# Kernel tuning notes

Hardware: AMD Instinct MI355X
Metric: run time of the kernel (lower is better)

Reference implementation:

```python
import jax, jax.numpy as jnp
import numpy as np

B, N, K = 4, 4096, 9
EPS = 1e-5

def _bn(y, g, b, axes):
    # BatchNorm forward with batch statistics; channel axis = 1
    m = y.mean(axis=axes, keepdims=True)
    v = y.var(axis=axes, keepdims=True)
    shape = [1] * y.ndim
    shape[1] = -1
    return (y - m) * jax.lax.rsqrt(v + EPS) * g.reshape(shape) + b.reshape(shape)

def _knn(x, k):
    # x: (B, C, N) -> neighbor indices (B, N, k), self-loops excluded
    x2 = jnp.sum(x * x, axis=1)  # (B, N)
    d = x2[:, :, None] + x2[:, None, :] - 2.0 * jnp.einsum('bcn,bcm->bnm', x, x)
    n = d.shape[-1]
    d = d + jnp.eye(n, dtype=d.dtype) * 1e10  # exclude self (self_loop=False)
    return jax.lax.top_k(-d, k)[1]  # (B, N, k)

def _edge_conv(x, idx, w, g, b):
    # EdgeConv: edge feature [x_i, x_j - x_i] -> 1x1 conv -> BN -> ReLU -> max over neighbors
    # x: (B, C, N); idx: (B, N, K); w: (O, 2C)
    xj = jnp.take_along_axis(x[:, :, None, :], idx[:, None, :, :], axis=3)  # (B,C,N,K)
    xi = x[:, :, :, None]
    e = jnp.concatenate([jnp.broadcast_to(xi, xj.shape), xj - xi], axis=1)  # (B,2C,N,K)
    y = jnp.einsum('oc,bcnk->bonk', w, e)
    y = jax.nn.relu(_bn(y, g, b, (0, 2, 3)))
    return y.max(axis=3)  # (B, O, N)

def setup_inputs():
    key = jax.random.key(0)
    ks = jax.random.split(key, 10)
    rn = lambda k, s: jax.random.normal(k, s, dtype=jnp.float32) * 0.1
    return {
        'x': jax.random.normal(ks[0], (B, 3, N), dtype=jnp.float32),
        'coords': jax.random.normal(ks[1], (B, 3, N), dtype=jnp.float32),
        'w1': rn(ks[2], (64, 6)), 'g1': jnp.ones(64), 'b1': jnp.zeros(64),
        'w2': rn(ks[3], (128, 128)), 'g2': jnp.ones(128), 'b2': jnp.zeros(128),
        'w3': rn(ks[4], (256, 256)), 'g3': jnp.ones(256), 'b3': jnp.zeros(256),
        'w4': rn(ks[5], (256, 512)), 'g4': jnp.ones(256), 'b4': jnp.zeros(256),
        'dec_w': rn(ks[6], (48, 64)), 'dec_g': jnp.ones(48), 'dec_b': jnp.zeros(48),
        'fus_w': rn(ks[7], (256, 304)),
        'cls_w1': rn(ks[8], (256, 512)), 'cls_g': jnp.ones(256), 'cls_b': jnp.zeros(256),
        'cls_w2': rn(ks[9], (40, 256)),
    }

def reference(x, coords, w1, g1, b1, w2, g2, b2, w3, g3, b3, w4, g4, b4,
              dec_w, dec_g, dec_b, fus_w, cls_w1, cls_g, cls_b, cls_w2):
    idx = _knn(x, K)                            # graph built once from input coords
    out1 = _edge_conv(x, idx, w1, g1, b1)       # (B, 64, N)  low_level_feats
    out = _edge_conv(out1, idx, w2, g2, b2)     # (B, 128, N)
    out = _edge_conv(out, idx, w3, g3, b3)      # (B, 256, N)
    out = _edge_conv(out, idx, w4, g4, b4)      # (B, 256, N)
    # Decoder (coords is accepted but unused, as in the torch module)
    low = jax.nn.relu(_bn(jnp.einsum('oc,bcn->bon', dec_w, out1), dec_g, dec_b, (0, 2)))  # (B,48,N)
    fused = jnp.einsum('oc,bcn->bon', fus_w, jnp.concatenate([out, low], axis=1))          # (B,256,N)
    h = jnp.concatenate([fused.max(axis=2, keepdims=True),
                         fused.mean(axis=2, keepdims=True)], axis=1)                        # (B,512,1)
    h = jax.nn.relu(_bn(jnp.einsum('oc,bcn->bon', cls_w1, h), cls_g, cls_b, (0, 2)))       # (B,256,1)
    logits = jnp.einsum('oc,bcn->bon', cls_w2, h).squeeze(-1)                               # (B,40)
    return logits
```

## Files before the change

kernel.cpp:

```cpp
#include <hip/hip_runtime.h>

#define BB 4
#define NN 4096
#define KK 9
#define NPTS (BB * NN)
#define EPSF 1e-5f

typedef short short8 __attribute__((ext_vector_type(8)));
typedef float f32x4 __attribute__((ext_vector_type(4)));

__device__ __forceinline__ unsigned short f2bf(float f) {
    unsigned u = __float_as_uint(f);
    unsigned r = (u + 0x7fffu + ((u >> 16) & 1u)) >> 16;
    return (unsigned short)r;
}
__device__ __forceinline__ float bf2f(unsigned short h) {
    return __uint_as_float(((unsigned)h) << 16);
}
__device__ __forceinline__ unsigned fmapu(float f) {
    unsigned u = __float_as_uint(f);
    return (u & 0x80000000u) ? ~u : (u | 0x80000000u);
}
__device__ __forceinline__ float funmap(unsigned m) {
    return (m & 0x80000000u) ? __uint_as_float(m & 0x7fffffffu) : __uint_as_float(~m);
}


__global__ __launch_bounds__(256) void knn_kernel(const float4* __restrict__ xt4, int* __restrict__ idx) {
    __shared__ float4 tile[32][9];
    __shared__ float smin[8][33];
    __shared__ float stauf[8];
    __shared__ int scnt[8];
    __shared__ unsigned long long spk[8][128];
    int tid = threadIdx.x;
    int q = tid & 7;
    int ch = tid >> 3;
    int blk = blockIdx.x;
    int b = blk >> 9;
    int qbase = (blk & 511) << 3;
    int n = qbase + q;
    const float4* xb = xt4 + (b << 12);
    float4 p = xb[n];
    float px2 = -2.0f * p.x, py2 = -2.0f * p.y, pz2 = -2.0f * p.z;
    if (tid < 8) scnt[tid] = 0;

    int lch = tid >> 3, li = tid & 7;
    float mn = 3.0e38f;

    for (int t0 = 0; t0 < 4096; t0 += 256) {
        __syncthreads();
        tile[lch][li] = xb[t0 + tid];
        __syncthreads();
        int mbase = t0 + ch * 8;
#pragma unroll
        for (int i = 0; i < 8; i += 4) {
            float4 c0 = tile[ch][i];
            float4 c1 = tile[ch][i + 1];
            float4 c2 = tile[ch][i + 2];
            float4 c3 = tile[ch][i + 3];
            float d0 = fmaf(px2, c0.x, fmaf(py2, c0.y, fmaf(pz2, c0.z, p.w + c0.w)));
            float d1 = fmaf(px2, c1.x, fmaf(py2, c1.y, fmaf(pz2, c1.z, p.w + c1.w)));
            float d2 = fmaf(px2, c2.x, fmaf(py2, c2.y, fmaf(pz2, c2.z, p.w + c2.w)));
            float d3 = fmaf(px2, c3.x, fmaf(py2, c3.y, fmaf(pz2, c3.z, p.w + c3.w)));
            int m = mbase + i;
            d0 = (m == n) ? 3.0e37f : d0;
            d1 = (m + 1 == n) ? 3.0e37f : d1;
            d2 = (m + 2 == n) ? 3.0e37f : d2;
            d3 = (m + 3 == n) ? 3.0e37f : d3;
            mn = fminf(mn, fminf(fminf(d0, d1), fminf(d2, d3)));
        }
    }
    smin[q][ch] = mn;
    __syncthreads();

    {
        int r = 0;
#pragma unroll 8
        for (int c = 0; c < 32; c++) {
            float u = smin[q][c];
            r += (u < mn || (u == mn && c < ch)) ? 1 : 0;
        }
        if (r == 8) stauf[q] = mn;
    }
    __syncthreads();
    float tau = stauf[q];

    for (int t0 = 0; t0 < 4096; t0 += 256) {
        __syncthreads();
        tile[lch][li] = xb[t0 + tid];
        __syncthreads();
        int mbase = t0 + ch * 8;
#pragma unroll
        for (int i = 0; i < 8; i += 4) {
            float4 c0 = tile[ch][i];
            float4 c1 = tile[ch][i + 1];
            float4 c2 = tile[ch][i + 2];
            float4 c3 = tile[ch][i + 3];
            float d0 = fmaf(px2, c0.x, fmaf(py2, c0.y, fmaf(pz2, c0.z, p.w + c0.w)));
            float d1 = fmaf(px2, c1.x, fmaf(py2, c1.y, fmaf(pz2, c1.z, p.w + c1.w)));
            float d2 = fmaf(px2, c2.x, fmaf(py2, c2.y, fmaf(pz2, c2.z, p.w + c2.w)));
            float d3 = fmaf(px2, c3.x, fmaf(py2, c3.y, fmaf(pz2, c3.z, p.w + c3.w)));
            int m = mbase + i;
            d0 = (m == n) ? 3.0e37f : d0;
            d1 = (m + 1 == n) ? 3.0e37f : d1;
            d2 = (m + 2 == n) ? 3.0e37f : d2;
            d3 = (m + 3 == n) ? 3.0e37f : d3;
            if (fminf(fminf(d0, d1), fminf(d2, d3)) <= tau) {
                if (d0 <= tau) {
                    int slot = atomicAdd(&scnt[q], 1);
                    if (slot < 128)
                        spk[q][slot] = (((unsigned long long)__float_as_uint(fmaxf(d0, 0.f))) << 32) | (unsigned)(m);
                }
                if (d1 <= tau) {
                    int slot = atomicAdd(&scnt[q], 1);
                    if (slot < 128)
                        spk[q][slot] = (((unsigned long long)__float_as_uint(fmaxf(d1, 0.f))) << 32) | (unsigned)(m + 1);
                }
                if (d2 <= tau) {
                    int slot = atomicAdd(&scnt[q], 1);
                    if (slot < 128)
                        spk[q][slot] = (((unsigned long long)__float_as_uint(fmaxf(d2, 0.f))) << 32) | (unsigned)(m + 2);
                }
                if (d3 <= tau) {
                    int slot = atomicAdd(&scnt[q], 1);
                    if (slot < 128)
                        spk[q][slot] = (((unsigned long long)__float_as_uint(fmaxf(d3, 0.f))) << 32) | (unsigned)(m + 3);
                }
            }
        }
    }
    __syncthreads();

    int cnt = scnt[q];
    cnt = (cnt > 128) ? 128 : cnt;
    size_t obase = ((size_t)(b << 12) + qbase + q) * KK;
    for (int s = ch; s < cnt; s += 32) {
        unsigned long long e = spk[q][s];
        int r = 0;
        for (int c = 0; c < cnt; c++) r += (spk[q][c] < e) ? 1 : 0;
        if (r < KK) idx[obase + r] = (int)(unsigned)e;
    }
}

__global__ void wprep_all_kernel(const float* __restrict__ x, const float* __restrict__ w1,
                                 const float* __restrict__ w2, const float* __restrict__ w3,
                                 const float* __restrict__ w4, const float* __restrict__ fw,
                                 float4* __restrict__ xt4,
                                 float* __restrict__ wc1, float* __restrict__ wc2,
                                 unsigned short* __restrict__ wc3h, unsigned short* __restrict__ wc3l,
                                 unsigned short* __restrict__ wc4h, unsigned short* __restrict__ wc4l,
                                 unsigned short* __restrict__ fwh, unsigned short* __restrict__ fwl,
                                 double* __restrict__ stats, unsigned* __restrict__ pmaxU,
                                 double* __restrict__ psum) {
    int i0 = blockIdx.x * 256 + threadIdx.x;
    if (i0 < 96256) stats[i0] = 0.0;
    if (i0 < 1024) { pmaxU[i0] = 0u; psum[i0] = 0.0; }
    int i = i0;
    if (i < 192) {
        int o = i / 3, c = i - o * 3;
        float a = w1[o * 6 + c], b = w1[o * 6 + 3 + c];
        wc1[o * 3 + c] = a - b;
        wc1[(64 + o) * 3 + c] = b;
        return;
    }
    i -= 192;
    if (i < 8192) {
        int o = i / 64, c = i - o * 64;
        float a = w2[o * 128 + c], b = w2[o * 128 + 64 + c];
        wc2[o * 64 + c] = a - b;
        wc2[(128 + o) * 64 + c] = b;
        return;
    }
    i -= 8192;
    if (i < 32768) {
        int o = i / 128, c = i - o * 128;
        float a = w3[o * 256 + c], b = w3[o * 256 + 128 + c];
        float vA = a - b;
        unsigned short h = f2bf(vA);
        wc3h[o * 128 + c] = h;
        wc3l[o * 128 + c] = f2bf(vA - bf2f(h));
        unsigned short h2 = f2bf(b);
        wc3h[(size_t)(256 + o) * 128 + c] = h2;
        wc3l[(size_t)(256 + o) * 128 + c] = f2bf(b - bf2f(h2));
        return;
    }
    i -= 32768;
    if (i < 65536) {
        int o = i / 256, c = i - o * 256;
        float a = w4[o * 512 + c], b = w4[o * 512 + 256 + c];
        float vA = a - b;
        unsigned short h = f2bf(vA);
        wc4h[o * 256 + c] = h;
        wc4l[o * 256 + c] = f2bf(vA - bf2f(h));
        unsigned short h2 = f2bf(b);
        wc4h[(size_t)(256 + o) * 256 + c] = h2;
        wc4l[(size_t)(256 + o) * 256 + c] = f2bf(b - bf2f(h2));
        return;
    }
    i -= 65536;
    if (i < 81920) {
        int o = i / 320, c = i - o * 320;
        float v = (c < 304) ? fw[o * 304 + c] : 0.f;
        unsigned short h = f2bf(v);
        fwh[i] = h;
        fwl[i] = f2bf(v - bf2f(h));
        return;
    }
    i -= 81920;
    if (i < NPTS) {
        int b = i >> 12, n = i & 4095;
        float x0 = x[(b * 3 + 0) * NN + n];
        float x1 = x[(b * 3 + 1) * NN + n];
        float x2 = x[(b * 3 + 2) * NN + n];
        float s = x0 * x0 + x1 * x1 + x2 * x2;
        xt4[i] = make_float4(x0, x1, x2, s);
    }
}

template <int K_, int LDA>
__global__ __launch_bounds__(256) void gemm_kernel(const float* __restrict__ A,
                                                   const float* __restrict__ Bw,
                                                   float* __restrict__ OutB,
                                                   unsigned short* __restrict__ OutZ,
                                                   int CBASE, int ldoB, int ldoZ) {
    constexpr int BK = 16;
    constexpr int LDS_S = 132;
    __shared__ float sA[BK * LDS_S];
    __shared__ float sB[BK * LDS_S];
    int tid = threadIdx.x;
    int m0 = blockIdx.x * 128;
    int n0 = blockIdx.y * 128;
    int lrow = tid >> 2;
    int kq = (tid & 3) * 4;
    int tm = (tid & 15) * 8;
    int tn = (tid >> 4) * 8;

    float acc[8][8];
#pragma unroll
    for (int i = 0; i < 8; i++)
#pragma unroll
        for (int j = 0; j < 8; j++) acc[i][j] = 0.f;

    for (int k0 = 0; k0 < K_; k0 += BK) {
#pragma unroll
        for (int h = 0; h < 2; h++) {
            int r = lrow + h * 64;
            float4 va = *(const float4*)(A + (size_t)(m0 + r) * LDA + k0 + kq);
            sA[(kq + 0) * LDS_S + r] = va.x;
            sA[(kq + 1) * LDS_S + r] = va.y;
            sA[(kq + 2) * LDS_S + r] = va.z;
            sA[(kq + 3) * LDS_S + r] = va.w;
            float4 vb = *(const float4*)(Bw + (size_t)(n0 + r) * K_ + k0 + kq);
            sB[(kq + 0) * LDS_S + r] = vb.x;
            sB[(kq + 1) * LDS_S + r] = vb.y;
            sB[(kq + 2) * LDS_S + r] = vb.z;
            sB[(kq + 3) * LDS_S + r] = vb.w;
        }
        __syncthreads();
#pragma unroll 4
        for (int k = 0; k < BK; k++) {
            float4 a0 = *(const float4*)(sA + k * LDS_S + tm);
            float4 a1 = *(const float4*)(sA + k * LDS_S + tm + 4);
            float4 b0 = *(const float4*)(sB + k * LDS_S + tn);
            float4 b1 = *(const float4*)(sB + k * LDS_S + tn + 4);
            float av[8] = {a0.x, a0.y, a0.z, a0.w, a1.x, a1.y, a1.z, a1.w};
            float bv[8] = {b0.x, b0.y, b0.z, b0.w, b1.x, b1.y, b1.z, b1.w};
#pragma unroll
            for (int i = 0; i < 8; i++)
#pragma unroll
                for (int j = 0; j < 8; j++) acc[i][j] = fmaf(av[i], bv[j], acc[i][j]);
        }
        __syncthreads();
    }
    if (n0 < CBASE) {
#pragma unroll
        for (int i = 0; i < 8; i++) {
            float4 o0 = make_float4(acc[i][0], acc[i][1], acc[i][2], acc[i][3]);
            float4 o1 = make_float4(acc[i][4], acc[i][5], acc[i][6], acc[i][7]);
            float* orow = OutB + (size_t)(m0 + tm + i) * ldoB + n0 + tn;
            *(float4*)(orow) = o0;
            *(float4*)(orow + 4) = o1;
        }
    } else {
        int zc = n0 - CBASE;
#pragma unroll
        for (int i = 0; i < 8; i++) {
            unsigned* zrow = (unsigned*)(OutZ + (size_t)(m0 + tm + i) * ldoZ + zc + tn);
#pragma unroll
            for (int j = 0; j < 4; j++)
                zrow[j] = (unsigned)f2bf(acc[i][2 * j]) | ((unsigned)f2bf(acc[i][2 * j + 1]) << 16);
        }
    }
}

template <int K_>
__global__ __launch_bounds__(256) void gemm_mfma2_kernel(const unsigned short* __restrict__ Ah,
                                                         const unsigned short* __restrict__ Al,
                                                         const unsigned short* __restrict__ Bh,
                                                         const unsigned short* __restrict__ Bl,
                                                         float* __restrict__ OutB,
                                                         unsigned short* __restrict__ OutZ,
                                                         int CBASE, int ldoB, int ldoZ) {
    constexpr int LR = 40;
    __shared__ unsigned short sAh[128 * LR];
    __shared__ unsigned short sAl[128 * LR];
    __shared__ unsigned short sBh[128 * LR];
    __shared__ unsigned short sBl[128 * LR];
    int tid = threadIdx.x;
    int wave = tid >> 6, lane = tid & 63;
    int r16 = lane & 15, quad = lane >> 4;
    int wm = (wave & 1) << 6, wn = (wave >> 1) << 6;
    int m0 = blockIdx.x * 128;
    int n0 = blockIdx.y * 128;
    int sr0 = tid >> 2;
    int sp0 = (tid & 3) * 8;
    const unsigned short* gAh = Ah + (size_t)(m0 + sr0) * K_ + sp0;
    const unsigned short* gAl = Al + (size_t)(m0 + sr0) * K_ + sp0;
    const unsigned short* gBh = Bh + (size_t)(n0 + sr0) * K_ + sp0;
    const unsigned short* gBl = Bl + (size_t)(n0 + sr0) * K_ + sp0;
    const size_t gstep = (size_t)64 * K_;
    unsigned short* lA0h = sAh + sr0 * LR + sp0;
    unsigned short* lA1h = lA0h + 64 * LR;
    unsigned short* lA0l = sAl + sr0 * LR + sp0;
    unsigned short* lA1l = lA0l + 64 * LR;
    unsigned short* lB0h = sBh + sr0 * LR + sp0;
    unsigned short* lB1h = lB0h + 64 * LR;
    unsigned short* lB0l = sBl + sr0 * LR + sp0;
    unsigned short* lB1l = lB0l + 64 * LR;

    f32x4 acc[4][4];
#pragma unroll
    for (int i = 0; i < 4; i++)
#pragma unroll
        for (int j = 0; j < 4; j++) acc[i][j] = (f32x4){0.f, 0.f, 0.f, 0.f};

    for (int k0 = 0; k0 < K_; k0 += 32) {
        __syncthreads();
        *(short8*)lA0h = *(const short8*)(gAh + k0);
        *(short8*)lA1h = *(const short8*)(gAh + gstep + k0);
        *(short8*)lA0l = *(const short8*)(gAl + k0);
        *(short8*)lA1l = *(const short8*)(gAl + gstep + k0);
        *(short8*)lB0h = *(const short8*)(gBh + k0);
        *(short8*)lB1h = *(const short8*)(gBh + gstep + k0);
        *(short8*)lB0l = *(const short8*)(gBl + k0);
        *(short8*)lB1l = *(const short8*)(gBl + gstep + k0);
        __syncthreads();
        short8 bh[4], bl[4];
#pragma unroll
        for (int j = 0; j < 4; j++) {
            bh[j] = *(const short8*)(sBh + (wn + j * 16 + r16) * LR + quad * 8);
            bl[j] = *(const short8*)(sBl + (wn + j * 16 + r16) * LR + quad * 8);
        }
#pragma unroll
        for (int i = 0; i < 4; i++) {
            short8 ah = *(const short8*)(sAh + (wm + i * 16 + r16) * LR + quad * 8);
            short8 al = *(const short8*)(sAl + (wm + i * 16 + r16) * LR + quad * 8);
#pragma unroll
            for (int j = 0; j < 4; j++) {
                acc[i][j] = __builtin_amdgcn_mfma_f32_16x16x32_bf16(ah, bh[j], acc[i][j], 0, 0, 0);
                acc[i][j] = __builtin_amdgcn_mfma_f32_16x16x32_bf16(ah, bl[j], acc[i][j], 0, 0, 0);
                acc[i][j] = __builtin_amdgcn_mfma_f32_16x16x32_bf16(al, bh[j], acc[i][j], 0, 0, 0);
            }
        }
    }

    int orow = quad * 4;
    if (n0 < CBASE) {
#pragma unroll
        for (int i = 0; i < 4; i++) {
#pragma unroll
            for (int v = 0; v < 4; v++) {
                float* prow = OutB + (size_t)(m0 + wm + i * 16 + orow + v) * ldoB + n0 + wn + r16;
#pragma unroll
                for (int j = 0; j < 4; j++) prow[j * 16] = acc[i][j][v];
            }
        }
    } else {
        int zc = n0 - CBASE;
#pragma unroll
        for (int i = 0; i < 4; i++) {
#pragma unroll
            for (int v = 0; v < 4; v++) {
                unsigned short* prow = OutZ + (size_t)(m0 + wm + i * 16 + orow + v) * ldoZ + zc + wn + r16;
#pragma unroll
                for (int j = 0; j < 4; j++) prow[j * 16] = f2bf(acc[i][j][v]);
            }
        }
    }
}

template <int K_>
__global__ __launch_bounds__(256) void gemm_mfma_red2_kernel(const unsigned short* __restrict__ Ah,
                                                             const unsigned short* __restrict__ Al,
                                                             const unsigned short* __restrict__ Bh,
                                                             const unsigned short* __restrict__ Bl,
                                                             unsigned* __restrict__ pmaxU,
                                                             double* __restrict__ psum) {
    constexpr int LR = 40;
    __shared__ unsigned short sAh[128 * LR];
    __shared__ unsigned short sAl[128 * LR];
    __shared__ unsigned short sBh[128 * LR];
    __shared__ unsigned short sBl[128 * LR];
    int tid = threadIdx.x;
    int wave = tid >> 6, lane = tid & 63;
    int r16 = lane & 15, quad = lane >> 4;
    int wm = (wave & 1) << 6, wn = (wave >> 1) << 6;
    int m0 = blockIdx.x * 128;
    int n0 = blockIdx.y * 128;
    int sr0 = tid >> 2;
    int sp0 = (tid & 3) * 8;
    const unsigned short* gAh = Ah + (size_t)(m0 + sr0) * K_ + sp0;
    const unsigned short* gAl = Al + (size_t)(m0 + sr0) * K_ + sp0;
    const unsigned short* gBh = Bh + (size_t)(n0 + sr0) * K_ + sp0;
    const unsigned short* gBl = Bl + (size_t)(n0 + sr0) * K_ + sp0;
    const size_t gstep = (size_t)64 * K_;
    unsigned short* lA0h = sAh + sr0 * LR + sp0;
    unsigned short* lA1h = lA0h + 64 * LR;
    unsigned short* lA0l = sAl + sr0 * LR + sp0;
    unsigned short* lA1l = lA0l + 64 * LR;
    unsigned short* lB0h = sBh + sr0 * LR + sp0;
    unsigned short* lB1h = lB0h + 64 * LR;
    unsigned short* lB0l = sBl + sr0 * LR + sp0;
    unsigned short* lB1l = lB0l + 64 * LR;

    f32x4 acc[4][4];
#pragma unroll
    for (int i = 0; i < 4; i++)
#pragma unroll
        for (int j = 0; j < 4; j++) acc[i][j] = (f32x4){0.f, 0.f, 0.f, 0.f};

    for (int k0 = 0; k0 < K_; k0 += 32) {
        __syncthreads();
        *(short8*)lA0h = *(const short8*)(gAh + k0);
        *(short8*)lA1h = *(const short8*)(gAh + gstep + k0);
        *(short8*)lA0l = *(const short8*)(gAl + k0);
        *(short8*)lA1l = *(const short8*)(gAl + gstep + k0);
        *(short8*)lB0h = *(const short8*)(gBh + k0);
        *(short8*)lB1h = *(const short8*)(gBh + gstep + k0);
        *(short8*)lB0l = *(const short8*)(gBl + k0);
        *(short8*)lB1l = *(const short8*)(gBl + gstep + k0);
        __syncthreads();
        short8 bh[4], bl[4];
#pragma unroll
        for (int j = 0; j < 4; j++) {
            bh[j] = *(const short8*)(sBh + (wn + j * 16 + r16) * LR + quad * 8);
            bl[j] = *(const short8*)(sBl + (wn + j * 16 + r16) * LR + quad * 8);
        }
#pragma unroll
        for (int i = 0; i < 4; i++) {
            short8 ah = *(const short8*)(sAh + (wm + i * 16 + r16) * LR + quad * 8);
            short8 al = *(const short8*)(sAl + (wm + i * 16 + r16) * LR + quad * 8);
#pragma unroll
            for (int j = 0; j < 4; j++) {
                acc[i][j] = __builtin_amdgcn_mfma_f32_16x16x32_bf16(ah, bh[j], acc[i][j], 0, 0, 0);
                acc[i][j] = __builtin_amdgcn_mfma_f32_16x16x32_bf16(ah, bl[j], acc[i][j], 0, 0, 0);
                acc[i][j] = __builtin_amdgcn_mfma_f32_16x16x32_bf16(al, bh[j], acc[i][j], 0, 0, 0);
            }
        }
    }

    int batch = (blockIdx.x * 128) >> 12;
#pragma unroll
    for (int j = 0; j < 4; j++) {
        float mx = -3.0e38f, sm = 0.f;
#pragma unroll
        for (int i = 0; i < 4; i++) {
#pragma unroll
            for (int v = 0; v < 4; v++) {
                float val = acc[i][j][v];
                mx = fmaxf(mx, val);
                sm += val;
            }
        }
        mx = fmaxf(mx, __shfl_xor(mx, 16));
        mx = fmaxf(mx, __shfl_xor(mx, 32));
        sm += __shfl_xor(sm, 16);
        sm += __shfl_xor(sm, 32);
        if (quad == 0) {
            int col = n0 + wn + j * 16 + r16;
            atomicMax(&pmaxU[batch * 256 + col], fmapu(mx));
            atomicAdd(&psum[batch * 256 + col], (double)sm);
        }
    }
}

__global__ __launch_bounds__(256) void gather1_kernel(const float4* __restrict__ xt4,
                                                      const int* __restrict__ idxb,
                                                      const float* __restrict__ wc1,
                                                      float* __restrict__ ymax,
                                                      double* __restrict__ stats) {
    __shared__ float swc[384];
    __shared__ float reds[4][64], reds2[4][64];
    int tid = threadIdx.x;
    for (int e = tid; e < 384; e += 256) swc[e] = wc1[e];
    __syncthreads();
    int t = tid & 63, p = tid >> 6;
    int n = blockIdx.x * 4 + p;
    int bbase = n & ~4095;
    float4 xn = xt4[n];
    float4 xj[KK];
#pragma unroll
    for (int k = 0; k < KK; k++) {
        int nbk = bbase + idxb[n * KK + k];
        xj[k] = xt4[nbk];
    }
    float a0 = swc[t * 3], a1 = swc[t * 3 + 1], a2 = swc[t * 3 + 2];
    float b0 = swc[(64 + t) * 3], b1 = swc[(64 + t) * 3 + 1], b2 = swc[(64 + t) * 3 + 2];
    float base = xn.x * a0 + xn.y * a1 + xn.z * a2;
    float mx = -3.0e38f, s = 0.f, s2 = 0.f;
#pragma unroll
    for (int k = 0; k < KK; k++) {
        float z = xj[k].x * b0 + xj[k].y * b1 + xj[k].z * b2;
        float v = base + z;
        mx = fmaxf(mx, v);
        s += v;
        s2 += v * v;
    }
    ymax[(size_t)n * 64 + t] = mx;
    reds[p][t] = s;
    reds2[p][t] = s2;
    __syncthreads();
    if (p == 0) {
        double ds = (double)reds[0][t] + (double)reds[1][t] + (double)reds[2][t] + (double)reds[3][t];
        double ds2 = (double)reds2[0][t] + (double)reds2[1][t] + (double)reds2[2][t] + (double)reds2[3][t];
        int part = blockIdx.x & 63;
        atomicAdd(&stats[part * 64 + t], ds);
        atomicAdd(&stats[64 * 64 + part * 64 + t], ds2);
    }
}

template <int COUT>
__global__ __launch_bounds__(256) void gather_kernel(const float* __restrict__ Gb,
                                                     const unsigned short* __restrict__ Gz,
                                                     const int* __restrict__ idxb,
                                                     float* __restrict__ ymax,
                                                     double* __restrict__ stats) {
    __shared__ float reds[4][64], reds2[4][64];
    int t = threadIdx.x & 63;
    int p = threadIdx.x >> 6;
    int blk = blockIdx.x;
    int xcd = blk & 7, grp = blk >> 3;
    int batch = xcd >> 1;
    int n = (batch << 12) + (((grp << 1) | (xcd & 1)) << 2) + p;
    int bbase = n & ~4095;
    int nb[KK];
#pragma unroll
    for (int k = 0; k < KK; k++) nb[k] = bbase + idxb[n * KK + k];
    const float* gb = Gb + (size_t)n * COUT;
    int part = blk & 63;
#pragma unroll 1
    for (int u = 0; u < COUT / 64; u++) {
        int o = t + u * 64;
        float base = gb[o];
        float mx = -3.0e38f, s = 0.f, s2 = 0.f;
#pragma unroll
        for (int k = 0; k < KK; k++) {
            float v = base + bf2f(Gz[(size_t)nb[k] * COUT + o]);
            mx = fmaxf(mx, v);
            s += v;
            s2 += v * v;
        }
        ymax[(size_t)n * COUT + o] = mx;
        reds[p][t] = s;
        reds2[p][t] = s2;
        __syncthreads();
        if (p == 0) {
            double ds = (double)reds[0][t] + (double)reds[1][t] + (double)reds[2][t] + (double)reds[3][t];
            double ds2 = (double)reds2[0][t] + (double)reds2[1][t] + (double)reds2[2][t] + (double)reds2[3][t];
            atomicAdd(&stats[part * COUT + o], ds);
            atomicAdd(&stats[64 * COUT + part * COUT + o], ds2);
        }
        __syncthreads();
    }
}

template <int COUT>
__global__ void finalize_kernel(const double* __restrict__ stats, const float* __restrict__ g,
                                const float* __restrict__ bias, float* __restrict__ ss,
                                float count) {
    int o = threadIdx.x;
    if (o >= COUT) return;
    double s = 0.0, s2 = 0.0;
    for (int p = 0; p < 64; p++) {
        s += stats[p * COUT + o];
        s2 += stats[64 * COUT + p * COUT + o];
    }
    double m = s / (double)count;
    double var = s2 / (double)count - m * m;
    float scale = g[o] * rsqrtf((float)var + EPSF);
    ss[o] = scale;
    ss[COUT + o] = bias[o] - (float)m * scale;
}

__global__ __launch_bounds__(256) void apply1dec_kernel(const float* __restrict__ ymax,
                                                        const float* __restrict__ ss,
                                                        const float* __restrict__ decw,
                                                        float* __restrict__ act1, float* __restrict__ z,
                                                        double* __restrict__ stats) {
    __shared__ __align__(16) float sx[4][64];
    __shared__ float sz[4][48];
    int t = threadIdx.x & 63, p = threadIdx.x >> 6;
    int n = blockIdx.x * 4 + p;
    size_t i = (size_t)n * 64 + t;
    float s = ss[t], sh = ss[64 + t];
    float r = fmaxf(fmaf(s, ymax[i], sh), 0.f);
    act1[i] = r;
    sx[p][t] = r;
    __syncthreads();
    if (t < 48) {
        const float* wr = decw + t * 64;
        float acc = 0.f;
#pragma unroll
        for (int c = 0; c < 64; c += 4) {
            float4 wv = *(const float4*)(wr + c);
            float4 xv = *(const float4*)(&sx[p][c]);
            acc += wv.x * xv.x + wv.y * xv.y + wv.z * xv.z + wv.w * xv.w;
        }
        z[(size_t)n * 48 + t] = acc;
        sz[p][t] = acc;
    }
    __syncthreads();
    if (p == 0 && t < 48) {
        double ds = 0.0, ds2 = 0.0;
#pragma unroll
        for (int pp = 0; pp < 4; pp++) {
            double a = (double)sz[pp][t];
            ds += a;
            ds2 += a * a;
        }
        int part = blockIdx.x & 63;
        atomicAdd(&stats[part * 48 + t], ds);
        atomicAdd(&stats[64 * 48 + part * 48 + t], ds2);
    }
}

template <int COUT, int LDO>
__global__ void apply_split_kernel(const float* __restrict__ ymax, const float* __restrict__ ss,
                                   unsigned short* __restrict__ outh,
                                   unsigned short* __restrict__ outl) {
    int i = blockIdx.x * 256 + threadIdx.x;
    int o = i & (COUT - 1);
    int n = i / COUT;
    float s = ss[o], sh = ss[COUT + o];
    float r = fmaxf(fmaf(s, ymax[i], sh), 0.f);
    unsigned short h = f2bf(r);
    size_t a = (size_t)n * LDO + o;
    outh[a] = h;
    outl[a] = f2bf(r - bf2f(h));
}

__global__ __launch_bounds__(320) void applyfused_kernel(const float* __restrict__ ymax,
                                                         const float* __restrict__ ss4,
                                                         const float* __restrict__ zdec,
                                                         const float* __restrict__ ssD,
                                                         unsigned short* __restrict__ fh,
                                                         unsigned short* __restrict__ fl) {
    int n = blockIdx.x;
    int o = threadIdx.x;
    float r = 0.f;
    if (o < 256) {
        float s = ss4[o], sh = ss4[256 + o];
        r = fmaxf(fmaf(s, ymax[(size_t)n * 256 + o], sh), 0.f);
    } else if (o < 304) {
        int oo = o - 256;
        float s = ssD[oo], sh = ssD[48 + oo];
        r = fmaxf(fmaf(s, zdec[(size_t)n * 48 + oo], sh), 0.f);
    }
    unsigned short h = f2bf(r);
    size_t a = (size_t)n * 320 + o;
    fh[a] = h;
    fl[a] = f2bf(r - bf2f(h));
}

__global__ __launch_bounds__(256) void cls1_kernel(const unsigned* __restrict__ pmaxU,
                                                   const double* __restrict__ psum,
                                                   const float* __restrict__ w1,
                                                   const float* __restrict__ g,
                                                   const float* __restrict__ bias,
                                                   float* __restrict__ h2o) {
    __shared__ __align__(16) float sh[4 * 512];
    __shared__ float red[16][17][4];
    int tid = threadIdx.x;
    int c = tid >> 4;
    int seg = tid & 15;
#pragma unroll
    for (int i = 0; i < 8; i++) {
        int e = tid + i * 256;
        int b2 = e >> 9, o = e & 511;
        sh[e] = (o < 256) ? funmap(pmaxU[b2 * 256 + o])
                          : (float)(psum[b2 * 256 + (o - 256)] * (1.0 / 4096.0));
    }
    __syncthreads();
    int t = blockIdx.x * 16 + c;
    const float* wr = w1 + (size_t)t * 512 + seg * 4;
    float a0 = 0.f, a1 = 0.f, a2 = 0.f, a3 = 0.f;
#pragma unroll
    for (int j = 0; j < 8; j++) {
        float4 wv = *(const float4*)(wr + j * 64);
        int so = seg * 4 + j * 64;
        float4 s0 = *(const float4*)(&sh[0 * 512 + so]);
        float4 s1 = *(const float4*)(&sh[1 * 512 + so]);
        float4 s2 = *(const float4*)(&sh[2 * 512 + so]);
        float4 s3 = *(const float4*)(&sh[3 * 512 + so]);
        a0 += wv.x * s0.x + wv.y * s0.y + wv.z * s0.z + wv.w * s0.w;
        a1 += wv.x * s1.x + wv.y * s1.y + wv.z * s1.z + wv.w * s1.w;
        a2 += wv.x * s2.x + wv.y * s2.y + wv.z * s2.z + wv.w * s2.w;
        a3 += wv.x * s3.x + wv.y * s3.y + wv.z * s3.z + wv.w * s3.w;
    }
    red[c][seg][0] = a0;
    red[c][seg][1] = a1;
    red[c][seg][2] = a2;
    red[c][seg][3] = a3;
    __syncthreads();
    if (seg == 0) {
        float y[4];
#pragma unroll
        for (int b2 = 0; b2 < 4; b2++) {
            float s = 0.f;
#pragma unroll
            for (int ss = 0; ss < 16; ss++) s += red[c][ss][b2];
            y[b2] = s;
        }
        float m = 0.25f * (y[0] + y[1] + y[2] + y[3]);
        float v = 0.25f * ((y[0] - m) * (y[0] - m) + (y[1] - m) * (y[1] - m) +
                           (y[2] - m) * (y[2] - m) + (y[3] - m) * (y[3] - m));
        float sc = g[t] * rsqrtf(v + EPSF);
        float shf = bias[t] - m * sc;
#pragma unroll
        for (int b2 = 0; b2 < 4; b2++) h2o[b2 * 256 + t] = fmaxf(fmaf(sc, y[b2], shf), 0.f);
    }
}

__global__ __launch_bounds__(256) void cls2_kernel(const float* __restrict__ h2o,
                                                   const float* __restrict__ w2,
                                                   float* __restrict__ out) {
    __shared__ __align__(16) float sh2[4 * 256];
    int t = threadIdx.x;
#pragma unroll
    for (int i = 0; i < 4; i++) sh2[t + i * 256] = h2o[t + i * 256];
    __syncthreads();
    if (t < 160) {
        int b2 = t / 40, j = t % 40;
        const float* wr2 = w2 + j * 256;
        float acc = 0.f;
        for (int c = 0; c < 256; c += 4) {
            float4 wv = *(const float4*)(wr2 + c);
            acc += wv.x * sh2[b2 * 256 + c] + wv.y * sh2[b2 * 256 + c + 1] +
                   wv.z * sh2[b2 * 256 + c + 2] + wv.w * sh2[b2 * 256 + c + 3];
        }
        out[b2 * 40 + j] = acc;
    }
}

extern "C" void kernel_launch(void* const* d_in, const int* in_sizes, int n_in,
                              void* d_out, int out_size, void* d_ws, size_t ws_size,
                              hipStream_t stream) {
    const float* x = (const float*)d_in[0];
    const float* w1 = (const float*)d_in[2];
    const float* g1 = (const float*)d_in[3];
    const float* b1 = (const float*)d_in[4];
    const float* w2 = (const float*)d_in[5];
    const float* g2 = (const float*)d_in[6];
    const float* b2 = (const float*)d_in[7];
    const float* w3 = (const float*)d_in[8];
    const float* g3 = (const float*)d_in[9];
    const float* b3 = (const float*)d_in[10];
    const float* w4 = (const float*)d_in[11];
    const float* g4 = (const float*)d_in[12];
    const float* b4 = (const float*)d_in[13];
    const float* dec_w = (const float*)d_in[14];
    const float* dec_g = (const float*)d_in[15];
    const float* dec_b = (const float*)d_in[16];
    const float* fus_w = (const float*)d_in[17];
    const float* cls_w1 = (const float*)d_in[18];
    const float* cls_g = (const float*)d_in[19];
    const float* cls_b = (const float*)d_in[20];
    const float* cls_w2 = (const float*)d_in[21];
    float* out = (float*)d_out;

    char* ws = (char*)d_ws;
    size_t cur = 0;
    auto alloc = [&](size_t bytes) -> void* {
        void* p = ws + cur;
        cur += (bytes + 255) & ~(size_t)255;
        return p;
    };
    const size_t STATS_DBL = 96256;
    double* stats = (double*)alloc(STATS_DBL * 8);
    const size_t OFF1 = 0, OFF2 = 8192, OFF3 = 24576, OFF4 = 57344, OFFD = 90112;
    double* psum2 = (double*)alloc(1024 * 8);
    unsigned* pmaxU = (unsigned*)alloc(1024 * 4);
    float* h2ws = (float*)alloc(1024 * 4);
    float4* xt4 = (float4*)alloc((size_t)NPTS * 16);
    int* idx = (int*)alloc((size_t)NPTS * KK * 4);
    float* act1 = (float*)alloc((size_t)NPTS * 64 * 4);
    unsigned short* act2h = (unsigned short*)alloc((size_t)NPTS * 128 * 2);
    unsigned short* act2l = (unsigned short*)alloc((size_t)NPTS * 128 * 2);
    unsigned short* act3h = (unsigned short*)alloc((size_t)NPTS * 256 * 2);
    unsigned short* act3l = (unsigned short*)alloc((size_t)NPTS * 256 * 2);
    unsigned short* actfh = (unsigned short*)alloc((size_t)NPTS * 320 * 2);
    unsigned short* actfl = (unsigned short*)alloc((size_t)NPTS * 320 * 2);
    float* Gb = (float*)alloc((size_t)NPTS * 256 * 4);
    unsigned short* Gz = (unsigned short*)alloc((size_t)NPTS * 256 * 2);
    float* zdec = (float*)alloc((size_t)NPTS * 48 * 4);
    float* ymax = (float*)alloc((size_t)NPTS * 256 * 4);
    float* ss = (float*)alloc(2048 * 4);
    const size_t SS1 = 0, SS2 = 128, SS3 = 384, SS4 = 896, SSD = 1408;
    float* wc1 = (float*)alloc(128 * 3 * 4);
    float* wc2 = (float*)alloc(256 * 64 * 4);
    unsigned short* wc3h = (unsigned short*)alloc((size_t)512 * 128 * 2);
    unsigned short* wc3l = (unsigned short*)alloc((size_t)512 * 128 * 2);
    unsigned short* wc4h = (unsigned short*)alloc((size_t)512 * 256 * 2);
    unsigned short* wc4l = (unsigned short*)alloc((size_t)512 * 256 * 2);
    unsigned short* fwh = (unsigned short*)alloc((size_t)256 * 320 * 2);
    unsigned short* fwl = (unsigned short*)alloc((size_t)256 * 320 * 2);

    wprep_all_kernel<<<801, 256, 0, stream>>>(x, w1, w2, w3, w4, fus_w, xt4, wc1, wc2, wc3h, wc3l,
                                              wc4h, wc4l, fwh, fwl, stats, pmaxU, psum2);
    knn_kernel<<<NPTS / 8, 256, 0, stream>>>(xt4, idx);

    gather1_kernel<<<NPTS / 4, 256, 0, stream>>>(xt4, idx, wc1, ymax, stats + OFF1);
    finalize_kernel<64><<<1, 64, 0, stream>>>(stats + OFF1, g1, b1, ss + SS1, 147456.f);
    apply1dec_kernel<<<NPTS / 4, 256, 0, stream>>>(ymax, ss + SS1, dec_w, act1, zdec, stats + OFFD);
    finalize_kernel<48><<<1, 64, 0, stream>>>(stats + OFFD, dec_g, dec_b, ss + SSD, 16384.f);

    gemm_kernel<64, 64><<<dim3(128, 2), 256, 0, stream>>>(act1, wc2, Gb, Gz, 128, 128, 128);
    gather_kernel<128><<<NPTS / 4, 256, 0, stream>>>(Gb, Gz, idx, ymax, stats + OFF2);
    finalize_kernel<128><<<1, 128, 0, stream>>>(stats + OFF2, g2, b2, ss + SS2, 147456.f);
    apply_split_kernel<128, 128><<<NPTS * 128 / 256, 256, 0, stream>>>(ymax, ss + SS2, act2h, act2l);

    gemm_mfma2_kernel<128><<<dim3(128, 4), 256, 0, stream>>>(act2h, act2l, wc3h, wc3l, Gb, Gz,
                                                             256, 256, 256);
    gather_kernel<256><<<NPTS / 4, 256, 0, stream>>>(Gb, Gz, idx, ymax, stats + OFF3);
    finalize_kernel<256><<<1, 256, 0, stream>>>(stats + OFF3, g3, b3, ss + SS3, 147456.f);
    apply_split_kernel<256, 256><<<NPTS * 256 / 256, 256, 0, stream>>>(ymax, ss + SS3, act3h, act3l);

    gemm_mfma2_kernel<256><<<dim3(128, 4), 256, 0, stream>>>(act3h, act3l, wc4h, wc4l, Gb, Gz,
                                                             256, 256, 256);
    gather_kernel<256><<<NPTS / 4, 256, 0, stream>>>(Gb, Gz, idx, ymax, stats + OFF4);
    finalize_kernel<256><<<1, 256, 0, stream>>>(stats + OFF4, g4, b4, ss + SS4, 147456.f);

    applyfused_kernel<<<NPTS, 320, 0, stream>>>(ymax, ss + SS4, zdec, ss + SSD, actfh, actfl);

    gemm_mfma_red2_kernel<320><<<dim3(128, 2), 256, 0, stream>>>(actfh, actfl, fwh, fwl, pmaxU,
                                                                 psum2);
    cls1_kernel<<<16, 256, 0, stream>>>(pmaxU, psum2, cls_w1, cls_g, cls_b, h2ws);
    cls2_kernel<<<1, 256, 0, stream>>>(h2ws, cls_w2, out);
}
```

Measured before the change: 346.2 us.

## Keep kNN candidates in registers and evaluate all 8 queries per thread

The kNN kernel now has each thread hold 16 candidate points in registers and compute distances against all 8 block queries, instead of tiling candidates through shared memory with one query per thread. This removes the shared-memory tile loads and the repeated __syncthreads in both passes. Per-chunk minima are reduced with wave shuffles before the threshold selection. It raises register pressure (16 float4 plus per-query arrays) and changes the atomic insertion pattern into the candidate lists.

```diff
diff --git a/kernel.cpp b/kernel.cpp
--- a/kernel.cpp
+++ b/kernel.cpp
@@ -27,110 +27,101 @@
 
 
 __global__ __launch_bounds__(256) void knn_kernel(const float4* __restrict__ xt4, int* __restrict__ idx) {
-    __shared__ float4 tile[32][9];
+    __shared__ float4 sq[8];
     __shared__ float smin[8][33];
     __shared__ float stauf[8];
     __shared__ int scnt[8];
     __shared__ unsigned long long spk[8][128];
     int tid = threadIdx.x;
-    int q = tid & 7;
-    int ch = tid >> 3;
     int blk = blockIdx.x;
     int b = blk >> 9;
     int qbase = (blk & 511) << 3;
-    int n = qbase + q;
     const float4* xb = xt4 + (b << 12);
-    float4 p = xb[n];
-    float px2 = -2.0f * p.x, py2 = -2.0f * p.y, pz2 = -2.0f * p.z;
-    if (tid < 8) scnt[tid] = 0;
-
-    int lch = tid >> 3, li = tid & 7;
-    float mn = 3.0e38f;
-
-    for (int t0 = 0; t0 < 4096; t0 += 256) {
-        __syncthreads();
-        tile[lch][li] = xb[t0 + tid];
-        __syncthreads();
-        int mbase = t0 + ch * 8;
-#pragma unroll
-        for (int i = 0; i < 8; i += 4) {
-            float4 c0 = tile[ch][i];
-            float4 c1 = tile[ch][i + 1];
-            float4 c2 = tile[ch][i + 2];
-            float4 c3 = tile[ch][i + 3];
-            float d0 = fmaf(px2, c0.x, fmaf(py2, c0.y, fmaf(pz2, c0.z, p.w + c0.w)));
-            float d1 = fmaf(px2, c1.x, fmaf(py2, c1.y, fmaf(pz2, c1.z, p.w + c1.w)));
-            float d2 = fmaf(px2, c2.x, fmaf(py2, c2.y, fmaf(pz2, c2.z, p.w + c2.w)));
-            float d3 = fmaf(px2, c3.x, fmaf(py2, c3.y, fmaf(pz2, c3.z, p.w + c3.w)));
-            int m = mbase + i;
-            d0 = (m == n) ? 3.0e37f : d0;
-            d1 = (m + 1 == n) ? 3.0e37f : d1;
-            d2 = (m + 2 == n) ? 3.0e37f : d2;
-            d3 = (m + 3 == n) ? 3.0e37f : d3;
-            mn = fminf(mn, fminf(fminf(d0, d1), fminf(d2, d3)));
-        }
-    }
-    smin[q][ch] = mn;
+    if (tid < 8) {
+        scnt[tid] = 0;
+        sq[tid] = xb[qbase + tid];
+    }
+    __syncthreads();
+
+    float4 cand[16];
+#pragma unroll
+    for (int j = 0; j < 16; j++) cand[j] = xb[j * 256 + tid];
+
+    float px2[8], py2[8], pz2[8], pw[8];
+#pragma unroll
+    for (int q = 0; q < 8; q++) {
+        float4 p = sq[q];
+        px2[q] = -2.0f * p.x;
+        py2[q] = -2.0f * p.y;
+        pz2[q] = -2.0f * p.z;
+        pw[q] = p.w;
+    }
+
+    float mnq[8];
+#pragma unroll
+    for (int q = 0; q < 8; q++) mnq[q] = 3.0e38f;
+#pragma unroll
+    for (int j = 0; j < 16; j++) {
+        float4 c = cand[j];
+        int m = j * 256 + tid;
+#pragma unroll
+        for (int q = 0; q < 8; q++) {
+            float d = fmaf(px2[q], c.x, fmaf(py2[q], c.y, fmaf(pz2[q], c.z, pw[q] + c.w)));
+            d = (m == qbase + q) ? 3.0e37f : d;
+            mnq[q] = fminf(mnq[q], d);
+        }
+    }
+
+#pragma unroll
+    for (int q = 0; q < 8; q++) {
+        float v = mnq[q];
+        v = fminf(v, __shfl_xor(v, 1));
+        v = fminf(v, __shfl_xor(v, 2));
+        v = fminf(v, __shfl_xor(v, 4));
+        mnq[q] = v;
+    }
+    if ((tid & 7) == 0) {
+        int chk = tid >> 3;
+#pragma unroll
+        for (int q = 0; q < 8; q++) smin[q][chk] = mnq[q];
+    }
     __syncthreads();
 
     {
+        int q2 = tid & 7, ch2 = tid >> 3;
+        float mn = smin[q2][ch2];
         int r = 0;
 #pragma unroll 8
         for (int c = 0; c < 32; c++) {
-            float u = smin[q][c];
-            r += (u < mn || (u == mn && c < ch)) ? 1 : 0;
-        }
-        if (r == 8) stauf[q] = mn;
-    }
-    __syncthreads();
-    float tau = stauf[q];
-
-    for (int t0 = 0; t0 < 4096; t0 += 256) {
-        __syncthreads();
-        tile[lch][li] = xb[t0 + tid];
-        __syncthreads();
-        int mbase = t0 + ch * 8;
-#pragma unroll
-        for (int i = 0; i < 8; i += 4) {
-            float4 c0 = tile[ch][i];
-            float4 c1 = tile[ch][i + 1];
-            float4 c2 = tile[ch][i + 2];
-            float4 c3 = tile[ch][i + 3];
-            float d0 = fmaf(px2, c0.x, fmaf(py2, c0.y, fmaf(pz2, c0.z, p.w + c0.w)));
-            float d1 = fmaf(px2, c1.x, fmaf(py2, c1.y, fmaf(pz2, c1.z, p.w + c1.w)));
-            float d2 = fmaf(px2, c2.x, fmaf(py2, c2.y, fmaf(pz2, c2.z, p.w + c2.w)));
-            float d3 = fmaf(px2, c3.x, fmaf(py2, c3.y, fmaf(pz2, c3.z, p.w + c3.w)));
-            int m = mbase + i;
-            d0 = (m == n) ? 3.0e37f : d0;
-            d1 = (m + 1 == n) ? 3.0e37f : d1;
-            d2 = (m + 2 == n) ? 3.0e37f : d2;
-            d3 = (m + 3 == n) ? 3.0e37f : d3;
-            if (fminf(fminf(d0, d1), fminf(d2, d3)) <= tau) {
-                if (d0 <= tau) {
-                    int slot = atomicAdd(&scnt[q], 1);
-                    if (slot < 128)
-                        spk[q][slot] = (((unsigned long long)__float_as_uint(fmaxf(d0, 0.f))) << 32) | (unsigned)(m);
-                }
-                if (d1 <= tau) {
-                    int slot = atomicAdd(&scnt[q], 1);
-                    if (slot < 128)
-                        spk[q][slot] = (((unsigned long long)__float_as_uint(fmaxf(d1, 0.f))) << 32) | (unsigned)(m + 1);
-                }
-                if (d2 <= tau) {
-                    int slot = atomicAdd(&scnt[q], 1);
-                    if (slot < 128)
-                        spk[q][slot] = (((unsigned long long)__float_as_uint(fmaxf(d2, 0.f))) << 32) | (unsigned)(m + 2);
-                }
-                if (d3 <= tau) {
-                    int slot = atomicAdd(&scnt[q], 1);
-                    if (slot < 128)
-                        spk[q][slot] = (((unsigned long long)__float_as_uint(fmaxf(d3, 0.f))) << 32) | (unsigned)(m + 3);
-                }
+            float u = smin[q2][c];
+            r += (u < mn || (u == mn && c < ch2)) ? 1 : 0;
+        }
+        if (r == 8) stauf[q2] = mn;
+    }
+    __syncthreads();
+
+    float tauv[8];
+#pragma unroll
+    for (int q = 0; q < 8; q++) tauv[q] = stauf[q];
+#pragma unroll
+    for (int j = 0; j < 16; j++) {
+        float4 c = cand[j];
+        int m = j * 256 + tid;
+#pragma unroll
+        for (int q = 0; q < 8; q++) {
+            float d = fmaf(px2[q], c.x, fmaf(py2[q], c.y, fmaf(pz2[q], c.z, pw[q] + c.w)));
+            d = (m == qbase + q) ? 3.0e37f : d;
+            if (d <= tauv[q]) {
+                int slot = atomicAdd(&scnt[q], 1);
+                if (slot < 128)
+                    spk[q][slot] = (((unsigned long long)__float_as_uint(fmaxf(d, 0.f))) << 32) | (unsigned)m;
             }
         }
     }
     __syncthreads();
 
+    int q = tid & 7;
+    int ch = tid >> 3;
     int cnt = scnt[q];
     cnt = (cnt > 128) ? 128 : cnt;
     size_t obase = ((size_t)(b << 12) + qbase + q) * KK;
```

New measurement: 348.2 us. No clear change (+0.6%).
